# Optimization experiments

Hardware: AMD Instinct MI355X
Metric: run time of the kernel (lower is better)

Reference implementation:

```python
import jax, jax.numpy as jnp
import numpy as np

EMBED_DIM = 1024
NUM_HEADS = 16
HEAD_DIM = EMBED_DIM // NUM_HEADS
ROPE_BASE = 10000.0


def _rope_angles(seq_len, head_dim):
    inv_freq = 1.0 / (ROPE_BASE ** (jnp.arange(0, head_dim, 2, dtype=jnp.float32) / head_dim))  # [D/2]
    pos = jnp.arange(seq_len, dtype=jnp.float32)
    ang = pos[:, None] * inv_freq[None, :]  # [S, D/2]
    return jnp.cos(ang), jnp.sin(ang)


def _apply_rope(t, cos, sin):
    # t: [B, H, S, D]; rotate-half convention
    d2 = t.shape[-1] // 2
    t1, t2 = t[..., :d2], t[..., d2:]
    return jnp.concatenate([t1 * cos - t2 * sin, t2 * cos + t1 * sin], axis=-1)


def setup_inputs() -> dict:
    key = jax.random.key(0)
    ks = jax.random.split(key, 6)
    B, S, E = 1, 4096, EMBED_DIM
    x = jax.random.normal(ks[0], (B, S, E), dtype=jnp.float32)
    # causal mask: True means masked-out (upper triangle above diagonal)
    mask = jnp.triu(jnp.ones((S, S), dtype=bool), k=1)[None, None, :, :]
    scale = 0.02
    wqkv_w = jax.random.normal(ks[1], (E, 3 * E), dtype=jnp.float32) * scale
    wqkv_b = jax.random.normal(ks[2], (3 * E,), dtype=jnp.float32) * scale
    out_w = jax.random.normal(ks[3], (E, E), dtype=jnp.float32) * scale
    out_b = jax.random.normal(ks[4], (E,), dtype=jnp.float32) * scale
    return {"x": x, "mask": mask, "wqkv_w": wqkv_w, "wqkv_b": wqkv_b, "out_w": out_w, "out_b": out_b}


def reference(x, mask, wqkv_w, wqkv_b, out_w, out_b):
    B, S, E = x.shape
    H, D = NUM_HEADS, HEAD_DIM
    qkv = x @ wqkv_w + wqkv_b  # [B, S, 3E]
    q, k, v = jnp.split(qkv, 3, axis=-1)
    # [B, S, E] -> [B, H, S, D]
    q = q.reshape(B, S, H, D).transpose(0, 2, 1, 3)
    k = k.reshape(B, S, H, D).transpose(0, 2, 1, 3)
    v = v.reshape(B, S, H, D).transpose(0, 2, 1, 3)
    cos, sin = _rope_angles(S, D)  # [S, D/2]
    q = _apply_rope(q, cos, sin)
    k = _apply_rope(k, cos, sin)
    scores = jnp.einsum('bhqd,bhkd->bhqk', q, k) * (D ** -0.5)  # [B, H, S, S]
    scores = jnp.where(mask[:, :, -S:, :], -jnp.inf, scores)
    weights = jax.nn.softmax(scores, axis=-1)
    ctx = jnp.einsum('bhqk,bhkd->bhqd', weights, v)  # [B, H, S, D]
    ctx = ctx.transpose(0, 2, 1, 3).reshape(B, S, E)
    return ctx @ out_w + out_b
```

## Files before the change

kernel.cpp:

```cpp
#include <hip/hip_runtime.h>
#include <hip/hip_bf16.h>
#include <math.h>

#define S_LEN 4096
#define EMB   1024
#define E3    3072
#define NH    16
#define HD    64

#define SLOTS_PER_HEAD 52
#define NSLOTS         832

typedef unsigned short u16;
typedef short          bfrag __attribute__((ext_vector_type(8)));
typedef float          ffrag __attribute__((ext_vector_type(4)));
typedef unsigned short us8   __attribute__((ext_vector_type(8)));
typedef unsigned short us4   __attribute__((ext_vector_type(4)));

__device__ __forceinline__ u16 f2bf(float f) {
    union { float f; unsigned u; } v; v.f = f;
    unsigned r = v.u + 0x7fffu + ((v.u >> 16) & 1u);
    return (u16)(r >> 16);
}
__device__ __forceinline__ float bf2f(u16 b) {
    union { unsigned u; float f; } v; v.u = ((unsigned)b) << 16;
    return v.f;
}
__device__ __forceinline__ unsigned pack_bf16_trunc(float lo, float hi) {
    union { float f; unsigned u; } a, b; a.f = lo; b.f = hi;
    return __builtin_amdgcn_perm(b.u, a.u, 0x07060302u);
}
__device__ __forceinline__ void gld16(const void* g, void* l) {
    __builtin_amdgcn_global_load_lds(
        (const __attribute__((address_space(1))) unsigned int*)g,
        (__attribute__((address_space(3))) unsigned int*)l, 16, 0, 0);
}

__global__ __launch_bounds__(256)
void rope_tab_kernel(float2* __restrict__ tab) {
    const int idx = blockIdx.x * 256 + threadIdx.x;
    const int s = idx >> 5, j = idx & 31;
    const float C = 13.287712379549449f / 32.0f;
    const float invf = exp2f(-(float)j * C);
    float sn, cs;
    sincosf((float)s * invf, &sn, &cs);
    tab[idx] = make_float2(cs, sn);
}

__global__ __launch_bounds__(256)
void cast_bf16_kernel(const float* __restrict__ in, u16* __restrict__ out) {
    const size_t i = ((size_t)blockIdx.x * 256 + threadIdx.x) * 8;
    float4 a = *(const float4*)(in + i);
    float4 b = *(const float4*)(in + i + 4);
    us8 o;
    o[0]=f2bf(a.x); o[1]=f2bf(a.y); o[2]=f2bf(a.z); o[3]=f2bf(a.w);
    o[4]=f2bf(b.x); o[5]=f2bf(b.y); o[6]=f2bf(b.z); o[7]=f2bf(b.w);
    *(us8*)(out + i) = o;
}

__global__ __launch_bounds__(256)
void transpose_cast_kernel(const float* __restrict__ in, u16* __restrict__ out,
                           int R, int C) {
    __shared__ u16 T[64][72];
    const int r0 = blockIdx.x * 64, c0 = blockIdx.y * 64;
    const int t = threadIdx.x;
    const int rr = t >> 2, cc = (t & 3) * 16;

    const float* ip = in + (size_t)(r0 + rr) * C + c0 + cc;
    u16 tmp[16];
    #pragma unroll
    for (int i4 = 0; i4 < 4; i4++) {
        float4 v = ((const float4*)ip)[i4];
        tmp[4*i4+0]=f2bf(v.x); tmp[4*i4+1]=f2bf(v.y);
        tmp[4*i4+2]=f2bf(v.z); tmp[4*i4+3]=f2bf(v.w);
    }
    #pragma unroll
    for (int i8 = 0; i8 < 2; i8++) {
        us8 vv;
        #pragma unroll
        for (int j = 0; j < 8; j++) vv[j] = tmp[8*i8+j];
        *(us8*)&T[rr][cc + 8*i8] = vv;
    }
    __syncthreads();

    const int oc = t >> 2, orr = (t & 3) * 16;
    u16 ot[16];
    #pragma unroll
    for (int j = 0; j < 16; j++) ot[j] = T[orr + j][oc];
    u16* op = out + (size_t)(c0 + oc) * R + r0 + orr;
    #pragma unroll
    for (int i8 = 0; i8 < 2; i8++) {
        us8 vv;
        #pragma unroll
        for (int j = 0; j < 8; j++) vv[j] = ot[8*i8+j];
        *(us8*)(op + 8*i8) = vv;
    }
}

template <int OUT_BF16, int NT, int ROPE, int MINW>
__global__ __launch_bounds__(256, MINW)
void gemm_bt_kernel(const u16* __restrict__ A, const u16* __restrict__ Bt,
                    const float* __restrict__ bias, void* __restrict__ Cv,
                    u16* __restrict__ vtp, const float2* __restrict__ rope,
                    int M, int N, int K) {
    constexpr int BN = 32 * NT;
    constexpr int WS = 16 * NT;
    __shared__ u16 As[2][128][32];
    __shared__ u16 Bs[2][BN][32];

    const int tid = threadIdx.x;
    const int w = tid >> 6, L = tid & 63;
    const int col = L & 15, quad = L >> 4;
    const int wm = w & 1, wn = w >> 1;
    const int m0 = blockIdx.x * 128, n0 = blockIdx.y * BN;

    ffrag acc[4][NT];
    #pragma unroll
    for (int a = 0; a < 4; a++)
        #pragma unroll
        for (int b = 0; b < NT; b++)
            #pragma unroll
            for (int r = 0; r < 4; r++) acc[a][b][r] = 0.f;

    const int srow = L >> 2;
    const int schk = L & 3;

    #pragma unroll
    for (int t = 0; t < 2; t++) {
        const int rg = (2 * w + t) * 16;
        gld16(A + (size_t)(m0 + rg + srow) * K + schk * 8, &As[0][rg][0]);
    }
    #pragma unroll
    for (int t = 0; t < NT / 2; t++) {
        const int rg = (w * (NT / 2) + t) * 16;
        gld16(Bt + (size_t)(n0 + rg + srow) * K + schk * 8, &Bs[0][rg][0]);
    }
    __syncthreads();

    int buf = 0;
    for (int k0 = 0; k0 < K; k0 += 32, buf ^= 1) {
        if (k0 + 32 < K) {
            #pragma unroll
            for (int t = 0; t < 2; t++) {
                const int rg = (2 * w + t) * 16;
                gld16(A + (size_t)(m0 + rg + srow) * K + k0 + 32 + schk * 8,
                      &As[buf ^ 1][rg][0]);
            }
            #pragma unroll
            for (int t = 0; t < NT / 2; t++) {
                const int rg = (w * (NT / 2) + t) * 16;
                gld16(Bt + (size_t)(n0 + rg + srow) * K + k0 + 32 + schk * 8,
                      &Bs[buf ^ 1][rg][0]);
            }
        }

        bfrag af[4], bf[NT];
        #pragma unroll
        for (int mt = 0; mt < 4; mt++)
            af[mt] = *(const bfrag*)&As[buf][64 * wm + 16 * mt + col][8 * quad];
        #pragma unroll
        for (int nt = 0; nt < NT; nt++)
            bf[nt] = *(const bfrag*)&Bs[buf][WS * wn + 16 * nt + col][8 * quad];
        #pragma unroll
        for (int mt = 0; mt < 4; mt++)
            #pragma unroll
            for (int nt = 0; nt < NT; nt++)
                acc[mt][nt] = __builtin_amdgcn_mfma_f32_16x16x32_bf16(
                    af[mt], bf[nt], acc[mt][nt], 0, 0, 0);

        __syncthreads();
    }

    float bv[NT];
    #pragma unroll
    for (int nt = 0; nt < NT; nt++) bv[nt] = bias[n0 + WS * wn + 16 * nt + col];

    if (ROPE && n0 < 2 * EMB) {
        const float SCq = (n0 < EMB) ? 0.125f * 1.44269504088896f : 1.0f;
        #pragma unroll
        for (int mt = 0; mt < 4; mt++) {
            #pragma unroll
            for (int r = 0; r < 4; r++) {
                const int mrow = m0 + 64 * wm + 16 * mt + 4 * quad + r;
                u16* cp = (u16*)Cv + (size_t)mrow * N + n0 + 64 * wn + col;
                #pragma unroll
                for (int pr = 0; pr < 2; pr++) {
                    const float2 t = rope[(size_t)mrow * 32 + col + 16 * pr];
                    const float cs = t.x, sn = t.y;
                    const float t1 = acc[mt][pr][r] + bv[pr];
                    const float t2 = acc[mt][pr + 2][r] + bv[pr + 2];
                    cp[16 * pr]      = f2bf((t1 * cs - t2 * sn) * SCq);
                    cp[16 * pr + 32] = f2bf((t2 * cs + t1 * sn) * SCq);
                }
            }
        }
    } else if (ROPE) {
        #pragma unroll
        for (int nt = 0; nt < NT; nt++) {
            const int dg = n0 - 2 * EMB + WS * wn + 16 * nt + col;
            #pragma unroll
            for (int mt = 0; mt < 4; mt++) {
                const int s0 = m0 + 64 * wm + 16 * mt + 4 * quad;
                us4 pk;
                #pragma unroll
                for (int r = 0; r < 4; r++) pk[r] = f2bf(acc[mt][nt][r] + bv[nt]);
                *(us4*)&vtp[(size_t)dg * S_LEN + s0] = pk;
            }
        }
    } else {
        #pragma unroll
        for (int mt = 0; mt < 4; mt++) {
            #pragma unroll
            for (int r = 0; r < 4; r++) {
                const int m = m0 + 64 * wm + 16 * mt + 4 * quad + r;
                #pragma unroll
                for (int nt = 0; nt < NT; nt++) {
                    const int n = n0 + WS * wn + 16 * nt + col;
                    const float val = acc[mt][nt][r] + bv[nt];
                    if (OUT_BF16) ((u16*)Cv)[(size_t)m * N + n] = f2bf(val);
                    else          ((float*)Cv)[(size_t)m * N + n] = val;
                }
            }
        }
    }
}

__global__ __launch_bounds__(256, 3)
void flash13_kernel(const u16* __restrict__ qkvb, const u16* __restrict__ vt,
                    u16* __restrict__ ctxb, u16* __restrict__ pO,
                    float* __restrict__ pL) {
    __shared__ u16 QP[4][32][64];
    __shared__ u16 Ks[2][64][64];
    __shared__ u16 Vs[2][64][64];

    const int id = blockIdx.x;
    const int x  = id & 7;
    const int tt = id >> 3;
    const int h  = x + 8 * (tt & 1);
    const int o  = tt >> 1;

    int qi, ch, nc;
    if (o < 30)      { qi = 31 - o / 3;        ch = o % 3;        nc = 3; }
    else if (o < 33) { qi = 10 - (o - 30);     ch = 0;            nc = 1; }
    else if (o < 55) { const int oo = o - 33;  qi = 21 - oo / 2;  ch = oo & 1; nc = 2; }
    else             { qi = 7 - (o - 55);      ch = 0;            nc = 1; }

    const int total = 2 * qi + 2;
    const int Lc    = (total + nc - 1) / nc;
    const int kt0   = ch * Lc;
    const int cnt   = min(Lc, total - kt0);
    const bool lastch = (kt0 + cnt == total);
    const int q0 = qi * 128;

    const int tid = threadIdx.x;
    const int w = tid >> 6, L = tid & 63;
    const int col = L & 15, quad = L >> 4;
    const int lr = L >> 3, lp = L & 7;
    const int lc = lp ^ lr;

    const bool domask = lastch;
    const int nwt = cnt - ((domask && w < 2) ? 1 : 0);

    const size_t kArow = (size_t)(16 * w + lr) * E3 + EMB + h * HD + lc * 8;
    const size_t vArow = ((size_t)h * HD + 16 * w + lr) * S_LEN + lc * 8;
    const size_t kt0off  = (size_t)kt0 * 64 * E3;
    const size_t vt0off  = (size_t)kt0 * 64;

    #pragma unroll
    for (int u = 0; u < 4; u++)
        gld16(qkvb + (size_t)(q0 + 32 * w + 8 * u + lr) * E3 + h * HD + lc * 8,
              &QP[w][8 * u][0]);
    #pragma unroll
    for (int u = 0; u < 2; u++) {
        gld16(qkvb + kArow + kt0off + (size_t)(8 * u) * E3,
              &Ks[0][16 * w + 8 * u][0]);
        gld16(vt + vArow + vt0off + (size_t)(8 * u) * S_LEN,
              &Vs[0][16 * w + 8 * u][0]);
    }
    __syncthreads();

    bfrag qf[2][2];
    #pragma unroll
    for (int i = 0; i < 2; i++)
        #pragma unroll
        for (int ks = 0; ks < 2; ks++)
            qf[i][ks] = *(const bfrag*)
                ((const char*)&QP[w][16 * i + col][0] +
                 16 * ((4 * ks + quad) ^ (col & 7)));

    bfrag ones;
    #pragma unroll
    for (int i = 0; i < 8; i++) ones[i] = (short)0x3F80;

    ffrag o_[4][2], ol[2];
    #pragma unroll
    for (int d4 = 0; d4 < 4; d4++)
        #pragma unroll
        for (int i = 0; i < 2; i++)
            #pragma unroll
            for (int r2 = 0; r2 < 4; r2++) o_[d4][i][r2] = 0.f;
    #pragma unroll
    for (int i = 0; i < 2; i++)
        #pragma unroll
        for (int r2 = 0; r2 < 4; r2++) ol[i][r2] = 0.f;

    #pragma unroll 1
    for (int t = 0; t < cnt; t++) {
        const int buf = t & 1;
        if (t + 1 < cnt) {
            const size_t ko = kArow + kt0off + (size_t)(t + 1) * 64 * E3;
            const size_t vo = vArow + vt0off + (size_t)(t + 1) * 64;
            #pragma unroll
            for (int u = 0; u < 2; u++) {
                gld16(qkvb + ko + (size_t)(8 * u) * E3,
                      &Ks[buf ^ 1][16 * w + 8 * u][0]);
                gld16(vt + vo + (size_t)(8 * u) * S_LEN,
                      &Vs[buf ^ 1][16 * w + 8 * u][0]);
            }
        }

        if (t < nwt) {
            ffrag st[4][2];
            #pragma unroll
            for (int t4 = 0; t4 < 4; t4++)
                #pragma unroll
                for (int i = 0; i < 2; i++)
                    #pragma unroll
                    for (int r2 = 0; r2 < 4; r2++) st[t4][i][r2] = 0.f;
            __builtin_amdgcn_s_setprio(1);
            #pragma unroll
            for (int ks = 0; ks < 2; ks++) {
                bfrag kf[4];
                #pragma unroll
                for (int t4 = 0; t4 < 4; t4++)
                    kf[t4] = *(const bfrag*)
                        &Ks[buf][16 * t4 + col][(((4 * ks + quad) ^ (col & 7)) * 8)];
                #pragma unroll
                for (int t4 = 0; t4 < 4; t4++)
                    #pragma unroll
                    for (int i = 0; i < 2; i++)
                        st[t4][i] = __builtin_amdgcn_mfma_f32_16x16x32_bf16(
                            kf[t4], qf[i][ks], st[t4][i], 0, 0, 0);
            }
            __builtin_amdgcn_s_setprio(0);

            if (domask && t == nwt - 1) {
                #pragma unroll
                for (int i = 0; i < 2; i++) {
                    const int qrel = 32 * (w & 1) + 16 * i + col;
                    #pragma unroll
                    for (int t4 = 0; t4 < 4; t4++) {
                        const int key0 = 16 * t4 + 4 * quad;
                        #pragma unroll
                        for (int r2 = 0; r2 < 4; r2++)
                            if (key0 + r2 > qrel) st[t4][i][r2] = -3.0e38f;
                    }
                }
            }

            #pragma unroll
            for (int i = 0; i < 2; i++) {
                const int prow = 16 * i + col;
                #pragma unroll
                for (int t4 = 0; t4 < 4; t4++) {
                    float pr[4];
                    #pragma unroll
                    for (int r2 = 0; r2 < 4; r2++) pr[r2] = exp2f(st[t4][i][r2]);
                    uint2 pk;
                    pk.x = pack_bf16_trunc(pr[0], pr[1]);
                    pk.y = pack_bf16_trunc(pr[2], pr[3]);
                    const int c2 = (2 * t4 + (quad >> 1)) ^ (col & 7);
                    *(uint2*)((char*)&QP[w][prow][0] + 16 * c2 + 8 * (quad & 1)) = pk;
                }
            }

            __builtin_amdgcn_s_setprio(1);
            #pragma unroll
            for (int ks = 0; ks < 2; ks++) {
                bfrag vf[4];
                #pragma unroll
                for (int d4 = 0; d4 < 4; d4++)
                    vf[d4] = *(const bfrag*)
                        &Vs[buf][16 * d4 + col][(((4 * ks + quad) ^ (col & 7)) * 8)];
                bfrag pf[2];
                #pragma unroll
                for (int i = 0; i < 2; i++)
                    pf[i] = *(const bfrag*)
                        ((const char*)&QP[w][16 * i + col][0] +
                         16 * ((4 * ks + quad) ^ (col & 7)));
                #pragma unroll
                for (int d4 = 0; d4 < 4; d4++)
                    #pragma unroll
                    for (int i = 0; i < 2; i++)
                        o_[d4][i] = __builtin_amdgcn_mfma_f32_16x16x32_bf16(
                            vf[d4], pf[i], o_[d4][i], 0, 0, 0);
                #pragma unroll
                for (int i = 0; i < 2; i++)
                    ol[i] = __builtin_amdgcn_mfma_f32_16x16x32_bf16(
                        ones, pf[i], ol[i], 0, 0, 0);
            }
            __builtin_amdgcn_s_setprio(0);
        }

        __syncthreads();
    }

    if (nc == 1) {
        #pragma unroll
        for (int i = 0; i < 2; i++) {
            const float inv = 1.0f / ol[i][0];
            const int qg = q0 + 32 * w + 16 * i + col;
            #pragma unroll
            for (int d4 = 0; d4 < 4; d4++) {
                us4 pk;
                #pragma unroll
                for (int r2 = 0; r2 < 4; r2++) pk[r2] = f2bf(o_[d4][i][r2] * inv);
                *(us4*)&ctxb[(size_t)qg * EMB + h * HD + 16 * d4 + 4 * quad] = pk;
            }
        }
    } else {
        const int jj = (qi <= 21) ? (qi - 11) * 2 + ch : 22 + (qi - 22) * 3 + ch;
        const int slot = h * SLOTS_PER_HEAD + jj;
        u16* po = pO + (size_t)slot * (128 * 64);
        float* pl = pL + slot * 128;
        #pragma unroll
        for (int i = 0; i < 2; i++) {
            const int qrow = 32 * w + 16 * i + col;
            #pragma unroll
            for (int d4 = 0; d4 < 4; d4++) {
                us4 pk;
                #pragma unroll
                for (int r2 = 0; r2 < 4; r2++) pk[r2] = f2bf(o_[d4][i][r2]);
                *(us4*)&po[(size_t)qrow * 64 + 16 * d4 + 4 * quad] = pk;
            }
            if (quad == 0) pl[qrow] = ol[i][0];
        }
    }
}

__global__ __launch_bounds__(256)
void combine_kernel(const u16* __restrict__ pO, const float* __restrict__ pL,
                    u16* __restrict__ ctxb) {
    const int g = blockIdx.x;
    const int h = g / 21, qq = g % 21;
    const int qi = 11 + qq;
    const int nc = (qi <= 21) ? 2 : 3;
    const int jj0 = (qi <= 21) ? (qi - 11) * 2 : 22 + (qi - 22) * 3;
    const int slot0 = h * SLOTS_PER_HEAD + jj0;

    const int t = threadIdx.x;
    const int q = t >> 1, dh = (t & 1) * 32;

    float l = 0.f;
    for (int p = 0; p < nc; p++) l += pL[(slot0 + p) * 128 + q];
    const float inv = 1.0f / l;

    u16* op = ctxb + (size_t)(qi * 128 + q) * EMB + h * HD + dh;

    #pragma unroll
    for (int j = 0; j < 4; j++) {
        float s[8] = {0.f, 0.f, 0.f, 0.f, 0.f, 0.f, 0.f, 0.f};
        for (int p = 0; p < nc; p++) {
            const us8 va = *(const us8*)
                (pO + ((size_t)(slot0 + p) * 128 + q) * 64 + dh + 8 * j);
            #pragma unroll
            for (int e = 0; e < 8; e++) s[e] += bf2f(va[e]);
        }
        us8 vo;
        #pragma unroll
        for (int e = 0; e < 8; e++) vo[e] = f2bf(s[e] * inv);
        *(us8*)(op + 8 * j) = vo;
    }
}

extern "C" void kernel_launch(void* const* d_in, const int* in_sizes, int n_in,
                              void* d_out, int out_size, void* d_ws, size_t ws_size,
                              hipStream_t stream) {
    const float* x      = (const float*)d_in[0];
    const float* wqkv_w = (const float*)d_in[2];
    const float* wqkv_b = (const float*)d_in[3];
    const float* out_w  = (const float*)d_in[4];
    const float* out_b  = (const float*)d_in[5];
    float* out = (float*)d_out;

    u16* qkvb = (u16*)d_ws;
    u16* ctxb = qkvb + (size_t)S_LEN * E3;
    u16* xb   = ctxb + (size_t)S_LEN * EMB;
    u16* wt   = xb   + (size_t)S_LEN * EMB;
    u16* owt  = wt   + (size_t)E3 * EMB;
    u16* vtb  = owt  + (size_t)EMB * EMB;

    u16*   pO = xb;
    float* pL = (float*)(xb + (size_t)NSLOTS * 128 * 64);

    float2* ropetab = (float2*)ctxb;

    dim3 blk(256);

    rope_tab_kernel<<<dim3(S_LEN * 32 / 256), blk, 0, stream>>>(ropetab);
    cast_bf16_kernel<<<dim3(S_LEN * EMB / (256 * 8)), blk, 0, stream>>>(x, xb);
    transpose_cast_kernel<<<dim3(EMB / 64, E3 / 64), blk, 0, stream>>>(
        wqkv_w, wt, EMB, E3);
    transpose_cast_kernel<<<dim3(EMB / 64, EMB / 64), blk, 0, stream>>>(
        out_w, owt, EMB, EMB);

    gemm_bt_kernel<1, 4, 1, 3><<<dim3(S_LEN / 128, E3 / 128), blk, 0, stream>>>(
        xb, wt, wqkv_b, qkvb, vtb, ropetab, S_LEN, E3, EMB);

    flash13_kernel<<<dim3(1008), blk, 0, stream>>>(qkvb, vtb, ctxb, pO, pL);
    combine_kernel<<<dim3(336), blk, 0, stream>>>(pO, pL, ctxb);

    gemm_bt_kernel<0, 2, 0, 2><<<dim3(S_LEN / 128, EMB / 64), blk, 0, stream>>>(
        ctxb, owt, out_b, out, nullptr, nullptr, S_LEN, EMB, EMB);
}
```

Measured before the change: 246.4 us.

## Fuse prep kernels into one launch and streamline flash inner loop

Merges the rope-table, input cast and two weight transpose-cast kernels into a single prep kernel that dispatches on block index, which removes three launches and their gaps. In the attention kernel, the score MFMAs now start from a zero fragment instead of zeroing the accumulators, the K loads are split per k-step, exp2f is replaced by raw v_exp_f32 inline asm, and the s_setprio hints are removed. Raw v_exp_f32 skips denormal and range handling, which is acceptable here because the inputs are softmax scores.

```diff
diff --git a/kernel.cpp b/kernel.cpp
--- a/kernel.cpp
+++ b/kernel.cpp
@@ -30,39 +30,22 @@
     union { float f; unsigned u; } a, b; a.f = lo; b.f = hi;
     return __builtin_amdgcn_perm(b.u, a.u, 0x07060302u);
 }
+__device__ __forceinline__ float fexp2(float x) {
+    float r;
+    asm("v_exp_f32 %0, %1" : "=v"(r) : "v"(x));
+    return r;
+}
 __device__ __forceinline__ void gld16(const void* g, void* l) {
     __builtin_amdgcn_global_load_lds(
         (const __attribute__((address_space(1))) unsigned int*)g,
         (__attribute__((address_space(3))) unsigned int*)l, 16, 0, 0);
 }
 
-__global__ __launch_bounds__(256)
-void rope_tab_kernel(float2* __restrict__ tab) {
-    const int idx = blockIdx.x * 256 + threadIdx.x;
-    const int s = idx >> 5, j = idx & 31;
-    const float C = 13.287712379549449f / 32.0f;
-    const float invf = exp2f(-(float)j * C);
-    float sn, cs;
-    sincosf((float)s * invf, &sn, &cs);
-    tab[idx] = make_float2(cs, sn);
-}
-
-__global__ __launch_bounds__(256)
-void cast_bf16_kernel(const float* __restrict__ in, u16* __restrict__ out) {
-    const size_t i = ((size_t)blockIdx.x * 256 + threadIdx.x) * 8;
-    float4 a = *(const float4*)(in + i);
-    float4 b = *(const float4*)(in + i + 4);
-    us8 o;
-    o[0]=f2bf(a.x); o[1]=f2bf(a.y); o[2]=f2bf(a.z); o[3]=f2bf(a.w);
-    o[4]=f2bf(b.x); o[5]=f2bf(b.y); o[6]=f2bf(b.z); o[7]=f2bf(b.w);
-    *(us8*)(out + i) = o;
-}
-
-__global__ __launch_bounds__(256)
-void transpose_cast_kernel(const float* __restrict__ in, u16* __restrict__ out,
-                           int R, int C) {
-    __shared__ u16 T[64][72];
-    const int r0 = blockIdx.x * 64, c0 = blockIdx.y * 64;
+__device__ __forceinline__ void transpose_body(const float* __restrict__ in,
+                                               u16* __restrict__ out,
+                                               int R, int C, int bx, int by,
+                                               u16 (*T)[72]) {
+    const int r0 = bx * 64, c0 = by * 64;
     const int t = threadIdx.x;
     const int rr = t >> 2, cc = (t & 3) * 16;
 
@@ -94,6 +77,38 @@
         #pragma unroll
         for (int j = 0; j < 8; j++) vv[j] = ot[8*i8+j];
         *(us8*)(op + 8*i8) = vv;
+    }
+}
+
+__global__ __launch_bounds__(256)
+void prep_kernel(const float* __restrict__ x, u16* __restrict__ xb,
+                 const float* __restrict__ wqkv_w, u16* __restrict__ wt,
+                 const float* __restrict__ out_w, u16* __restrict__ owt,
+                 float2* __restrict__ tab) {
+    __shared__ u16 T[64][72];
+    const int b = blockIdx.x;
+    if (b < 2048) {
+        const size_t i = ((size_t)b * 256 + threadIdx.x) * 8;
+        float4 a = *(const float4*)(x + i);
+        float4 c = *(const float4*)(x + i + 4);
+        us8 o;
+        o[0]=f2bf(a.x); o[1]=f2bf(a.y); o[2]=f2bf(a.z); o[3]=f2bf(a.w);
+        o[4]=f2bf(c.x); o[5]=f2bf(c.y); o[6]=f2bf(c.z); o[7]=f2bf(c.w);
+        *(us8*)(xb + i) = o;
+    } else if (b < 2816) {
+        const int bb = b - 2048;
+        transpose_body(wqkv_w, wt, EMB, E3, bb & 15, bb >> 4, T);
+    } else if (b < 3072) {
+        const int bb = b - 2816;
+        transpose_body(out_w, owt, EMB, EMB, bb & 15, bb >> 4, T);
+    } else {
+        const int idx = (b - 3072) * 256 + threadIdx.x;
+        const int s = idx >> 5, j = idx & 31;
+        const float C = 13.287712379549449f / 32.0f;
+        const float invf = exp2f(-(float)j * C);
+        float sn, cs;
+        sincosf((float)s * invf, &sn, &cs);
+        tab[idx] = make_float2(cs, sn);
     }
 }
 
@@ -226,7 +241,7 @@
 }
 
 __global__ __launch_bounds__(256, 3)
-void flash13_kernel(const u16* __restrict__ qkvb, const u16* __restrict__ vt,
+void flash14_kernel(const u16* __restrict__ qkvb, const u16* __restrict__ vt,
                     u16* __restrict__ ctxb, u16* __restrict__ pO,
                     float* __restrict__ pL) {
     __shared__ u16 QP[4][32][64];
@@ -291,6 +306,7 @@
     bfrag ones;
     #pragma unroll
     for (int i = 0; i < 8; i++) ones[i] = (short)0x3F80;
+    const ffrag zf = {0.f, 0.f, 0.f, 0.f};
 
     ffrag o_[4][2], ol[2];
     #pragma unroll
@@ -321,28 +337,27 @@
 
         if (t < nwt) {
             ffrag st[4][2];
+            bfrag kf[4];
             #pragma unroll
             for (int t4 = 0; t4 < 4; t4++)
+                kf[t4] = *(const bfrag*)
+                    &Ks[buf][16 * t4 + col][((quad ^ (col & 7)) * 8)];
+            #pragma unroll
+            for (int t4 = 0; t4 < 4; t4++)
                 #pragma unroll
                 for (int i = 0; i < 2; i++)
-                    #pragma unroll
-                    for (int r2 = 0; r2 < 4; r2++) st[t4][i][r2] = 0.f;
-            __builtin_amdgcn_s_setprio(1);
-            #pragma unroll
-            for (int ks = 0; ks < 2; ks++) {
-                bfrag kf[4];
-                #pragma unroll
-                for (int t4 = 0; t4 < 4; t4++)
-                    kf[t4] = *(const bfrag*)
-                        &Ks[buf][16 * t4 + col][(((4 * ks + quad) ^ (col & 7)) * 8)];
-                #pragma unroll
-                for (int t4 = 0; t4 < 4; t4++)
-                    #pragma unroll
-                    for (int i = 0; i < 2; i++)
-                        st[t4][i] = __builtin_amdgcn_mfma_f32_16x16x32_bf16(
-                            kf[t4], qf[i][ks], st[t4][i], 0, 0, 0);
-            }
-            __builtin_amdgcn_s_setprio(0);
+                    st[t4][i] = __builtin_amdgcn_mfma_f32_16x16x32_bf16(
+                        kf[t4], qf[i][0], zf, 0, 0, 0);
+            #pragma unroll
+            for (int t4 = 0; t4 < 4; t4++)
+                kf[t4] = *(const bfrag*)
+                    &Ks[buf][16 * t4 + col][(((4 + quad) ^ (col & 7)) * 8)];
+            #pragma unroll
+            for (int t4 = 0; t4 < 4; t4++)
+                #pragma unroll
+                for (int i = 0; i < 2; i++)
+                    st[t4][i] = __builtin_amdgcn_mfma_f32_16x16x32_bf16(
+                        kf[t4], qf[i][1], st[t4][i], 0, 0, 0);
 
             if (domask && t == nwt - 1) {
                 #pragma unroll
@@ -365,7 +380,7 @@
                 for (int t4 = 0; t4 < 4; t4++) {
                     float pr[4];
                     #pragma unroll
-                    for (int r2 = 0; r2 < 4; r2++) pr[r2] = exp2f(st[t4][i][r2]);
+                    for (int r2 = 0; r2 < 4; r2++) pr[r2] = fexp2(st[t4][i][r2]);
                     uint2 pk;
                     pk.x = pack_bf16_trunc(pr[0], pr[1]);
                     pk.y = pack_bf16_trunc(pr[2], pr[3]);
@@ -374,7 +389,6 @@
                 }
             }
 
-            __builtin_amdgcn_s_setprio(1);
             #pragma unroll
             for (int ks = 0; ks < 2; ks++) {
                 bfrag vf[4];
@@ -399,7 +413,6 @@
                     ol[i] = __builtin_amdgcn_mfma_f32_16x16x32_bf16(
                         ones, pf[i], ol[i], 0, 0, 0);
             }
-            __builtin_amdgcn_s_setprio(0);
         }
 
         __syncthreads();
@@ -497,17 +510,13 @@
 
     dim3 blk(256);
 
-    rope_tab_kernel<<<dim3(S_LEN * 32 / 256), blk, 0, stream>>>(ropetab);
-    cast_bf16_kernel<<<dim3(S_LEN * EMB / (256 * 8)), blk, 0, stream>>>(x, xb);
-    transpose_cast_kernel<<<dim3(EMB / 64, E3 / 64), blk, 0, stream>>>(
-        wqkv_w, wt, EMB, E3);
-    transpose_cast_kernel<<<dim3(EMB / 64, EMB / 64), blk, 0, stream>>>(
-        out_w, owt, EMB, EMB);
+    prep_kernel<<<dim3(3584), blk, 0, stream>>>(
+        x, xb, wqkv_w, wt, out_w, owt, ropetab);
 
     gemm_bt_kernel<1, 4, 1, 3><<<dim3(S_LEN / 128, E3 / 128), blk, 0, stream>>>(
         xb, wt, wqkv_b, qkvb, vtb, ropetab, S_LEN, E3, EMB);
 
-    flash13_kernel<<<dim3(1008), blk, 0, stream>>>(qkvb, vtb, ctxb, pO, pL);
+    flash14_kernel<<<dim3(1008), blk, 0, stream>>>(qkvb, vtb, ctxb, pO, pL);
     combine_kernel<<<dim3(336), blk, 0, stream>>>(pO, pL, ctxb);
 
     gemm_bt_kernel<0, 2, 0, 2><<<dim3(S_LEN / 128, EMB / 64), blk, 0, stream>>>(
```

Result: faster. 231.4 us (-6.1%).
